# Kernel optimization log

Measured on AMD Instinct MI355X. Metric: run time of the kernel, lower is better.

Reference implementation:

```python
import jax, jax.numpy as jnp
import numpy as np

B, S, H, E, V = 64, 2048, 1024, 512, 32000


def setup_inputs() -> dict:
    key = jax.random.key(0)
    ks = jax.random.split(key, 10)
    s = lambda k, shape, scale: jax.random.normal(k, shape, jnp.float32) * scale
    return {
        "input_batch": jax.random.randint(ks[0], (B,), 0, V),
        "prev_h": s(ks[1], (B, H), 0.1),
        "prev_c": s(ks[2], (B, H), 0.1),
        "encoder_outputs": s(ks[3], (S, B, H), 0.1),
        "emb_W": s(ks[4], (V, E), 0.02),           # nn.Embedding weight
        "attn_W": s(ks[5], (2 * H,), 0.02),        # nn.Linear(2H, 1) weight (flattened)
        "attn_b": jnp.zeros((), jnp.float32),
        "W_ih": s(ks[6], (4 * H, E + H), 0.02),    # LSTMCell weight_ih
        "W_hh": s(ks[7], (4 * H, H), 0.02),        # LSTMCell weight_hh
        "b_ih": jnp.zeros((4 * H,), jnp.float32),
        "b_hh": jnp.zeros((4 * H,), jnp.float32),
        "out_W": s(ks[8], (V, H), 0.02),           # linear_out weight
        "out_b": jnp.zeros((V,), jnp.float32),
    }


def reference(input_batch, prev_h, prev_c, encoder_outputs, emb_W, attn_W, attn_b,
              W_ih, W_hh, b_ih, b_hh, out_W, out_b):
    hid = prev_h.shape[1]
    emb = emb_W[input_batch]                                   # [B, E]

    # Additive attention score attn(cat(prev_h[i], enc[j,i])) vectorized:
    # score[b, s] = prev_h[b] . W[:H] + enc[s, b] . W[H:] + bias
    Wh, We = attn_W[:hid], attn_W[hid:]
    scores = (prev_h @ Wh)[:, None] + jnp.einsum("sbh,h->bs", encoder_outputs, We) + attn_b
    attn_weights = jax.nn.softmax(scores, axis=1)              # [B, S]

    # context = bmm(attn[B,1,S], enc^T[B,S,H]) -> [B, H]
    context = jnp.einsum("bs,sbh->bh", attn_weights, encoder_outputs)

    x = jnp.concatenate([emb, context], axis=1)                # [B, E+H]

    # LSTMCell step (PyTorch gate order: i, f, g, o)
    gates = x @ W_ih.T + b_ih + prev_h @ W_hh.T + b_hh         # [B, 4H]
    i, f, g, o = jnp.split(gates, 4, axis=1)
    i, f, o = jax.nn.sigmoid(i), jax.nn.sigmoid(f), jax.nn.sigmoid(o)
    g = jnp.tanh(g)
    cell = f * prev_c + i * g
    hidden = o * jnp.tanh(cell)

    logits = hidden @ out_W.T + out_b                          # [B, V]
    output = jax.nn.log_softmax(logits, axis=1)
    return output, hidden, cell, attn_weights
```

## Files before the change

kernel.cpp:

```cpp
#include <hip/hip_runtime.h>
#include <math.h>

#define B 64
#define S 2048
#define H 1024
#define E 512
#define V 32000
#define G4 4096
#define KX 1536
#define KC 2560

typedef __attribute__((ext_vector_type(8))) short short8v;
typedef __attribute__((ext_vector_type(4))) float f32x4;

__device__ __forceinline__ ushort f2bf(float f) {
    union { float f; unsigned u; } v; v.f = f;
    unsigned r = v.u + 0x7FFFu + ((v.u >> 16) & 1u);
    return (ushort)(r >> 16);
}

__global__ __launch_bounds__(256) void prep_kernel(const int* __restrict__ ib,
                                                   const float* __restrict__ emb_W,
                                                   const float* __restrict__ prev_h,
                                                   const float* __restrict__ attn_W,
                                                   float* __restrict__ hwh,
                                                   float* __restrict__ xT) {
    __shared__ float red[256];
    int t = threadIdx.x;
    if (blockIdx.x < 64) {
        int b = blockIdx.x;
        float4 p = *(const float4*)(prev_h + b * H + t * 4);
        float4 w = *(const float4*)(attn_W + t * 4);
        red[t] = p.x * w.x + p.y * w.y + p.z * w.z + p.w * w.w;
        __syncthreads();
        for (int s2 = 128; s2; s2 >>= 1) {
            if (t < s2) red[t] += red[t + s2];
            __syncthreads();
        }
        if (t == 0) hwh[b] = red[0];
    } else {
        int g = (blockIdx.x - 64) * 256 + t;
        if (g < E * B) {
            int b = g & 63, k = g >> 6;
            xT[k * B + b] = emb_W[(size_t)ib[b] * E + k];
        } else {
            int g2 = g - E * B;
            int b = g2 & 63, k = g2 >> 6;
            xT[(KX + k) * B + b] = prev_h[b * H + k];
        }
    }
}

__global__ __launch_bounds__(256) void fused_attn_kernel(const float* __restrict__ enc,
                                                         const float* __restrict__ attn_W,
                                                         const float* __restrict__ attn_b,
                                                         const float* __restrict__ hwh,
                                                         float* __restrict__ scores,
                                                         float* __restrict__ cpart,
                                                         float* __restrict__ mlc) {
    __shared__ float mw[4], lw[4];
    __shared__ float cbuf[4][1024];
    int t = threadIdx.x;
    int lane = t & 63, wid = t >> 6;
    int bx = blockIdx.x;
    int b = bx >> 5, chunk = bx & 31;
    int s0 = chunk * 64 + wid * 16;

    const float* We = attn_W + H;
    float4 we4[4];
#pragma unroll
    for (int c = 0; c < 4; ++c) we4[c] = *(const float4*)(We + c * 256 + lane * 4);
    float cst = hwh[b] + attn_b[0];

    float m = -INFINITY, l = 0.f;
    float4 ctx4[4] = {{0,0,0,0},{0,0,0,0},{0,0,0,0},{0,0,0,0}};

    const float* rowp = enc + (size_t)s0 * (B * H) + b * H + lane * 4;
    float4 e4[4];
#pragma unroll
    for (int c = 0; c < 4; ++c) e4[c] = *(const float4*)(rowp + c * 256);

    for (int i = 0; i < 16; ++i) {
        float4 cur[4];
#pragma unroll
        for (int c = 0; c < 4; ++c) cur[c] = e4[c];
        if (i < 15) {
            const float* np = rowp + (size_t)(i + 1) * (B * H);
#pragma unroll
            for (int c = 0; c < 4; ++c) e4[c] = *(const float4*)(np + c * 256);
        }
        float acc = 0.f;
#pragma unroll
        for (int c = 0; c < 4; ++c)
            acc += cur[c].x * we4[c].x + cur[c].y * we4[c].y +
                   cur[c].z * we4[c].z + cur[c].w * we4[c].w;
#pragma unroll
        for (int x = 32; x; x >>= 1) acc += __shfl_xor(acc, x);
        float score = acc + cst;
        if (lane == 0) scores[b * S + s0 + i] = score;
        float nm = fmaxf(m, score);
        float sc = expf(m - nm);
        float w = expf(score - nm);
        l = l * sc + w;
        m = nm;
#pragma unroll
        for (int c = 0; c < 4; ++c) {
            ctx4[c].x = ctx4[c].x * sc + w * cur[c].x;
            ctx4[c].y = ctx4[c].y * sc + w * cur[c].y;
            ctx4[c].z = ctx4[c].z * sc + w * cur[c].z;
            ctx4[c].w = ctx4[c].w * sc + w * cur[c].w;
        }
    }

    if (lane == 0) { mw[wid] = m; lw[wid] = l; }
    __syncthreads();
    float M = fmaxf(fmaxf(mw[0], mw[1]), fmaxf(mw[2], mw[3]));
    float L = lw[0] * expf(mw[0] - M) + lw[1] * expf(mw[1] - M) +
              lw[2] * expf(mw[2] - M) + lw[3] * expf(mw[3] - M);
    float msc = expf(m - M);
#pragma unroll
    for (int c = 0; c < 4; ++c) {
        float4 v = ctx4[c];
        v.x *= msc; v.y *= msc; v.z *= msc; v.w *= msc;
        *(float4*)&cbuf[wid][c * 256 + lane * 4] = v;
    }
    __syncthreads();
    if (wid == 0) {
#pragma unroll
        for (int c = 0; c < 4; ++c) {
            int h = c * 256 + lane * 4;
            float4 a0 = *(float4*)&cbuf[0][h];
            float4 a1 = *(float4*)&cbuf[1][h];
            float4 a2 = *(float4*)&cbuf[2][h];
            float4 a3 = *(float4*)&cbuf[3][h];
            float4 s4 = make_float4(a0.x + a1.x + a2.x + a3.x,
                                    a0.y + a1.y + a2.y + a3.y,
                                    a0.z + a1.z + a2.z + a3.z,
                                    a0.w + a1.w + a2.w + a3.w);
            *(float4*)(cpart + (size_t)(chunk * B + b) * H + h) = s4;
        }
    }
    if (t == 0) {
        mlc[(b * 32 + chunk) * 2] = M;
        mlc[(b * 32 + chunk) * 2 + 1] = L;
    }
}

__global__ __launch_bounds__(256) void attn_reduce_kernel(const float* __restrict__ cpart,
                                                          const float* __restrict__ mlc,
                                                          const float* __restrict__ scores,
                                                          float* __restrict__ xT,
                                                          float* __restrict__ mlf,
                                                          float* __restrict__ attn) {
    __shared__ float Ms[32], Ls[32];
    int b = blockIdx.x, t = threadIdx.x;
    if (t < 32) {
        Ms[t] = mlc[(b * 32 + t) * 2];
        Ls[t] = mlc[(b * 32 + t) * 2 + 1];
    }
    __syncthreads();
    float Mg = -INFINITY;
#pragma unroll
    for (int c = 0; c < 32; ++c) Mg = fmaxf(Mg, Ms[c]);
    float Lg = 0.f;
#pragma unroll
    for (int c = 0; c < 32; ++c) Lg += Ls[c] * expf(Ms[c] - Mg);
    float inv = 1.f / Lg;
    int h = t * 4;
    float4 acc = {0, 0, 0, 0};
    for (int c = 0; c < 32; ++c) {
        float w = expf(Ms[c] - Mg);
        float4 v = *(const float4*)(cpart + (size_t)(c * B + b) * H + h);
        acc.x += w * v.x; acc.y += w * v.y; acc.z += w * v.z; acc.w += w * v.w;
    }
    xT[(E + h) * B + b]     = acc.x * inv;
    xT[(E + h + 1) * B + b] = acc.y * inv;
    xT[(E + h + 2) * B + b] = acc.z * inv;
    xT[(E + h + 3) * B + b] = acc.w * inv;
    if (t == 0) { mlf[b * 2] = Mg; mlf[b * 2 + 1] = Lg; }
#pragma unroll
    for (int i = 0; i < 8; ++i) {
        int s = t + i * 256;
        attn[b * S + s] = expf(scores[b * S + s] - Mg) * inv;
    }
}

__global__ __launch_bounds__(256) void gates_gemm(const float* __restrict__ W_ih,
                                                  const float* __restrict__ W_hh,
                                                  const float* __restrict__ xT,
                                                  float* __restrict__ gpart) {
    __shared__ float Wt[64][68];
    __shared__ float Xt[64][68];
    int t = threadIdx.x;
    int rtile = blockIdx.x >> 3, ks = blockIdx.x & 7;
    int r0 = rtile * 64;
    int rr0 = (t >> 4) * 4;
    int c0 = (t & 15) * 4;
    int sv = t >> 4;
    int sk = (t & 15) * 4;
    float acc[4][4] = {{0.f}};
    for (int kt = 0; kt < 5; ++kt) {
        int kb = ks * 320 + kt * 64;
        const float* wbase;
        int wstride;
        if (kb < KX) { wbase = W_ih + kb; wstride = KX; }
        else         { wbase = W_hh + (kb - KX); wstride = H; }
        __syncthreads();
#pragma unroll
        for (int g = 0; g < 4; ++g) {
            int vv = sv + g * 16;
            *(float4*)&Wt[vv][sk] = *(const float4*)(wbase + (size_t)(r0 + vv) * wstride + sk);
            *(float4*)&Xt[vv][sk] = *(const float4*)(xT + (size_t)(kb + vv) * B + sk);
        }
        __syncthreads();
#pragma unroll
        for (int k0 = 0; k0 < 64; k0 += 4) {
            float w[4][4], x[4][4];
#pragma unroll
            for (int ri = 0; ri < 4; ++ri) *(float4*)w[ri] = *(const float4*)&Wt[rr0 + ri][k0];
#pragma unroll
            for (int kj = 0; kj < 4; ++kj) *(float4*)x[kj] = *(const float4*)&Xt[k0 + kj][c0];
#pragma unroll
            for (int kj = 0; kj < 4; ++kj)
#pragma unroll
                for (int ri = 0; ri < 4; ++ri)
#pragma unroll
                    for (int ci = 0; ci < 4; ++ci)
                        acc[ri][ci] += w[ri][kj] * x[kj][ci];
        }
    }
#pragma unroll
    for (int ri = 0; ri < 4; ++ri) {
        float4 o4 = make_float4(acc[ri][0], acc[ri][1], acc[ri][2], acc[ri][3]);
        *(float4*)(gpart + (size_t)ks * (G4 * B) + (size_t)(r0 + rr0 + ri) * B + c0) = o4;
    }
}

__global__ __launch_bounds__(256) void lstm_kernel(const float* __restrict__ gpart,
                                                   const float* __restrict__ b_ih,
                                                   const float* __restrict__ b_hh,
                                                   const float* __restrict__ prev_c,
                                                   float* __restrict__ hidden_out,
                                                   float* __restrict__ cell_out,
                                                   ushort* __restrict__ hb) {
    int t = blockIdx.x * 256 + threadIdx.x;
    int b = t & 63, h = t >> 6;
    float g[4];
#pragma unroll
    for (int q = 0; q < 4; ++q) {
        int r = h + q * H;
        float a = b_ih[r] + b_hh[r];
#pragma unroll
        for (int ks = 0; ks < 8; ++ks) a += gpart[(size_t)ks * (G4 * B) + r * B + b];
        g[q] = a;
    }
    float ig = 1.f / (1.f + expf(-g[0]));
    float fg = 1.f / (1.f + expf(-g[1]));
    float gg = tanhf(g[2]);
    float og = 1.f / (1.f + expf(-g[3]));
    float c = fg * prev_c[b * H + h] + ig * gg;
    float hd = og * tanhf(c);
    cell_out[b * H + h] = c;
    hidden_out[b * H + h] = hd;
    hb[b * H + h] = f2bf(hd);
}

__global__ __launch_bounds__(256) void logits_mfma(const float* __restrict__ W,
                                                   const float* __restrict__ ob,
                                                   const ushort* __restrict__ hb,
                                                   float* __restrict__ outl) {
    __shared__ ushort Wt[64 * 64];
    __shared__ ushort Bt[64 * 64];
    __shared__ float  Ct[64][68];
    int t = threadIdx.x;
    int lane = t & 63, wid = t >> 6;
    int v0 = blockIdx.x * 64;

    int srow = t >> 2;
    int sq = t & 3;

    f32x4 acc[4] = {{0.f,0.f,0.f,0.f},{0.f,0.f,0.f,0.f},{0.f,0.f,0.f,0.f},{0.f,0.f,0.f,0.f}};

    int r = lane & 15, g = lane >> 4;
    int arow = wid * 16 + r;
    int aswz = (arow & 7) << 4;
    unsigned abase = arow * 128;

    for (int kt = 0; kt < 16; ++kt) {
        int k0 = kt * 64;
        __syncthreads();
        {
            const float* src = W + (size_t)(v0 + srow) * H + k0 + sq * 16;
            float4 f0 = *(const float4*)(src + 0);
            float4 f1 = *(const float4*)(src + 4);
            float4 f2 = *(const float4*)(src + 8);
            float4 f3 = *(const float4*)(src + 12);
            short8v w0, w1;
            w0[0] = (short)f2bf(f0.x); w0[1] = (short)f2bf(f0.y);
            w0[2] = (short)f2bf(f0.z); w0[3] = (short)f2bf(f0.w);
            w0[4] = (short)f2bf(f1.x); w0[5] = (short)f2bf(f1.y);
            w0[6] = (short)f2bf(f1.z); w0[7] = (short)f2bf(f1.w);
            w1[0] = (short)f2bf(f2.x); w1[1] = (short)f2bf(f2.y);
            w1[2] = (short)f2bf(f2.z); w1[3] = (short)f2bf(f2.w);
            w1[4] = (short)f2bf(f3.x); w1[5] = (short)f2bf(f3.y);
            w1[6] = (short)f2bf(f3.z); w1[7] = (short)f2bf(f3.w);
            unsigned rb = srow * 128;
            unsigned sw = (srow & 7) << 4;
            *(short8v*)((char*)Wt + rb + ((sq * 32 + 0) ^ sw))  = w0;
            *(short8v*)((char*)Wt + rb + ((sq * 32 + 16) ^ sw)) = w1;
        }
        {
            const ushort* hsrc = hb + (size_t)srow * H + k0 + sq * 16;
            uint4 h0 = *(const uint4*)(hsrc);
            uint4 h1 = *(const uint4*)(hsrc + 8);
            unsigned rb = srow * 128;
            unsigned sw = (srow & 7) << 4;
            *(uint4*)((char*)Bt + rb + ((sq * 32 + 0) ^ sw))  = h0;
            *(uint4*)((char*)Bt + rb + ((sq * 32 + 16) ^ sw)) = h1;
        }
        __syncthreads();
#pragma unroll
        for (int kk = 0; kk < 2; ++kk) {
            unsigned koff = kk * 64 + g * 16;
            short8v a = *(short8v*)((char*)Wt + abase + (koff ^ aswz));
#pragma unroll
            for (int bt = 0; bt < 4; ++bt) {
                int brow = bt * 16 + r;
                short8v bb = *(short8v*)((char*)Bt + brow * 128 + (koff ^ ((brow & 7) << 4)));
                acc[bt] = __builtin_amdgcn_mfma_f32_16x16x32_bf16(a, bb, acc[bt], 0, 0, 0);
            }
        }
    }
    __syncthreads();
    float bias[4];
#pragma unroll
    for (int j = 0; j < 4; ++j) bias[j] = ob[v0 + wid * 16 + g * 4 + j];
#pragma unroll
    for (int bt = 0; bt < 4; ++bt)
#pragma unroll
        for (int j = 0; j < 4; ++j)
            Ct[bt * 16 + r][wid * 16 + g * 4 + j] = acc[bt][j] + bias[j];
    __syncthreads();
    int ob_ = t >> 2;
    int vq = (t & 3) * 16;
#pragma unroll
    for (int c = 0; c < 4; ++c)
        *(float4*)(outl + (size_t)ob_ * V + v0 + vq + c * 4) = *(float4*)&Ct[ob_][vq + c * 4];
}

__global__ __launch_bounds__(256) void lse_kernel(const float* __restrict__ lg,
                                                  float* __restrict__ c) {
    __shared__ float rm[256], rl[256];
    int b = blockIdx.x, t = threadIdx.x;
    const float4* row = (const float4*)(lg + (size_t)b * V);
    float m = -3.4e38f, l = 0.f;
    for (int i = t; i < V / 4; i += 256) {
        float4 x = row[i];
        float xm = fmaxf(fmaxf(x.x, x.y), fmaxf(x.z, x.w));
        float nm = fmaxf(m, xm);
        l = l * expf(m - nm) + expf(x.x - nm) + expf(x.y - nm) + expf(x.z - nm) + expf(x.w - nm);
        m = nm;
    }
    rm[t] = m; rl[t] = l; __syncthreads();
    for (int s2 = 128; s2; s2 >>= 1) {
        if (t < s2) {
            float m2 = rm[t + s2], l2 = rl[t + s2];
            float nm = fmaxf(rm[t], m2);
            rl[t] = rl[t] * expf(rm[t] - nm) + l2 * expf(m2 - nm);
            rm[t] = nm;
        }
        __syncthreads();
    }
    if (t == 0) c[b] = rm[0] + logf(rl[0]);
}

__global__ __launch_bounds__(256) void lsub_kernel(const float* __restrict__ c,
                                                   float* __restrict__ lg) {
    int g = blockIdx.x * 256 + threadIdx.x;
    int b = g / (V / 4), w = g - b * (V / 4);
    float4* p = (float4*)(lg + (size_t)b * V) + w;
    float4 x = *p;
    float cc = c[b];
    x.x -= cc; x.y -= cc; x.z -= cc; x.w -= cc;
    *p = x;
}

extern "C" void kernel_launch(void* const* d_in, const int* in_sizes, int n_in,
                              void* d_out, int out_size, void* d_ws, size_t ws_size,
                              hipStream_t stream) {
    const int*   ib      = (const int*)d_in[0];
    const float* prev_h  = (const float*)d_in[1];
    const float* prev_c  = (const float*)d_in[2];
    const float* enc     = (const float*)d_in[3];
    const float* emb_W   = (const float*)d_in[4];
    const float* attn_W  = (const float*)d_in[5];
    const float* attn_b  = (const float*)d_in[6];
    const float* W_ih    = (const float*)d_in[7];
    const float* W_hh    = (const float*)d_in[8];
    const float* b_ih    = (const float*)d_in[9];
    const float* b_hh    = (const float*)d_in[10];
    const float* out_W   = (const float*)d_in[11];
    const float* out_b   = (const float*)d_in[12];

    float* ws = (float*)d_ws;
    float* sc   = ws;
    float* hwh  = ws + 131072;
    float* xT   = ws + 131200;
    float* cp   = ws + 295040;
    float* gp   = cp;
    float* mlc  = ws + 2392192;
    float* mlf  = ws + 2396288;
    float* cvec = ws + 2396416;
    ushort* hb  = (ushort*)(ws + 2396480);

    float* out    = (float*)d_out;
    float* out_ls = out;
    float* out_h  = out + (size_t)B * V;
    float* out_c  = out_h + (size_t)B * H;
    float* out_a  = out_c + (size_t)B * H;

    hipLaunchKernelGGL(prep_kernel,        dim3(448),  dim3(256), 0, stream, ib, emb_W, prev_h, attn_W, hwh, xT);
    hipLaunchKernelGGL(fused_attn_kernel,  dim3(2048), dim3(256), 0, stream, enc, attn_W, attn_b, hwh, sc, cp, mlc);
    hipLaunchKernelGGL(attn_reduce_kernel, dim3(B),    dim3(256), 0, stream, cp, mlc, sc, xT, mlf, out_a);
    hipLaunchKernelGGL(gates_gemm,         dim3(512),  dim3(256), 0, stream, W_ih, W_hh, xT, gp);
    hipLaunchKernelGGL(lstm_kernel,        dim3(256),  dim3(256), 0, stream, gp, b_ih, b_hh, prev_c, out_h, out_c, hb);
    hipLaunchKernelGGL(logits_mfma,        dim3(500),  dim3(256), 0, stream, out_W, out_b, hb, out_ls);
    hipLaunchKernelGGL(lse_kernel,         dim3(B),    dim3(256), 0, stream, out_ls, cvec);
    hipLaunchKernelGGL(lsub_kernel,        dim3(2000), dim3(256), 0, stream, cvec, out_ls);
}
```

Measured before the change: 208.2 us.

## Fuse log-softmax partials into logits GEMM, widen attention reduce, use nontemporal loads

```diff
diff --git a/kernel.cpp b/kernel.cpp
--- a/kernel.cpp
+++ b/kernel.cpp
@@ -9,6 +9,7 @@
 #define G4 4096
 #define KX 1536
 #define KC 2560
+#define NVT 500
 
 typedef __attribute__((ext_vector_type(8))) short short8v;
 typedef __attribute__((ext_vector_type(4))) float f32x4;
@@ -17,6 +18,11 @@
     union { float f; unsigned u; } v; v.f = f;
     unsigned r = v.u + 0x7FFFu + ((v.u >> 16) & 1u);
     return (ushort)(r >> 16);
+}
+
+__device__ __forceinline__ float4 ntload4(const float* p) {
+    f32x4 v = __builtin_nontemporal_load((const f32x4*)p);
+    return make_float4(v[0], v[1], v[2], v[3]);
 }
 
 __global__ __launch_bounds__(256) void prep_kernel(const int* __restrict__ ib,
@@ -78,7 +84,7 @@
     const float* rowp = enc + (size_t)s0 * (B * H) + b * H + lane * 4;
     float4 e4[4];
 #pragma unroll
-    for (int c = 0; c < 4; ++c) e4[c] = *(const float4*)(rowp + c * 256);
+    for (int c = 0; c < 4; ++c) e4[c] = ntload4(rowp + c * 256);
 
     for (int i = 0; i < 16; ++i) {
         float4 cur[4];
@@ -87,7 +93,7 @@
         if (i < 15) {
             const float* np = rowp + (size_t)(i + 1) * (B * H);
 #pragma unroll
-            for (int c = 0; c < 4; ++c) e4[c] = *(const float4*)(np + c * 256);
+            for (int c = 0; c < 4; ++c) e4[c] = ntload4(np + c * 256);
         }
         float acc = 0.f;
 #pragma unroll
@@ -150,10 +156,11 @@
                                                           const float* __restrict__ mlc,
                                                           const float* __restrict__ scores,
                                                           float* __restrict__ xT,
-                                                          float* __restrict__ mlf,
                                                           float* __restrict__ attn) {
-    __shared__ float Ms[32], Ls[32];
-    int b = blockIdx.x, t = threadIdx.x;
+    __shared__ float Ms[32], Ls[32], Es[32];
+    int blk = blockIdx.x;
+    int b = blk >> 2, q = blk & 3;
+    int t = threadIdx.x;
     if (t < 32) {
         Ms[t] = mlc[(b * 32 + t) * 2];
         Ls[t] = mlc[(b * 32 + t) * 2 + 1];
@@ -162,25 +169,21 @@
     float Mg = -INFINITY;
 #pragma unroll
     for (int c = 0; c < 32; ++c) Mg = fmaxf(Mg, Ms[c]);
+    if (t < 32) Es[t] = expf(Ms[t] - Mg);
+    __syncthreads();
     float Lg = 0.f;
 #pragma unroll
-    for (int c = 0; c < 32; ++c) Lg += Ls[c] * expf(Ms[c] - Mg);
+    for (int c = 0; c < 32; ++c) Lg += Ls[c] * Es[c];
     float inv = 1.f / Lg;
-    int h = t * 4;
-    float4 acc = {0, 0, 0, 0};
-    for (int c = 0; c < 32; ++c) {
-        float w = expf(Ms[c] - Mg);
-        float4 v = *(const float4*)(cpart + (size_t)(c * B + b) * H + h);
-        acc.x += w * v.x; acc.y += w * v.y; acc.z += w * v.z; acc.w += w * v.w;
-    }
-    xT[(E + h) * B + b]     = acc.x * inv;
-    xT[(E + h + 1) * B + b] = acc.y * inv;
-    xT[(E + h + 2) * B + b] = acc.z * inv;
-    xT[(E + h + 3) * B + b] = acc.w * inv;
-    if (t == 0) { mlf[b * 2] = Mg; mlf[b * 2 + 1] = Lg; }
-#pragma unroll
-    for (int i = 0; i < 8; ++i) {
-        int s = t + i * 256;
+    int h = q * 256 + t;
+    float acc = 0.f;
+#pragma unroll 4
+    for (int c = 0; c < 32; ++c)
+        acc += Es[c] * cpart[(size_t)(c * B + b) * H + h];
+    xT[(E + h) * B + b] = acc * inv;
+#pragma unroll
+    for (int i = 0; i < 2; ++i) {
+        int s = q * 512 + i * 256 + t;
         attn[b * S + s] = expf(scores[b * S + s] - Mg) * inv;
     }
 }
@@ -268,7 +271,8 @@
 __global__ __launch_bounds__(256) void logits_mfma(const float* __restrict__ W,
                                                    const float* __restrict__ ob,
                                                    const ushort* __restrict__ hb,
-                                                   float* __restrict__ outl) {
+                                                   float* __restrict__ outl,
+                                                   float* __restrict__ lsp) {
     __shared__ ushort Wt[64 * 64];
     __shared__ ushort Bt[64 * 64];
     __shared__ float  Ct[64][68];
@@ -291,10 +295,10 @@
         __syncthreads();
         {
             const float* src = W + (size_t)(v0 + srow) * H + k0 + sq * 16;
-            float4 f0 = *(const float4*)(src + 0);
-            float4 f1 = *(const float4*)(src + 4);
-            float4 f2 = *(const float4*)(src + 8);
-            float4 f3 = *(const float4*)(src + 12);
+            float4 f0 = ntload4(src + 0);
+            float4 f1 = ntload4(src + 4);
+            float4 f2 = ntload4(src + 8);
+            float4 f3 = ntload4(src + 12);
             short8v w0, w1;
             w0[0] = (short)f2bf(f0.x); w0[1] = (short)f2bf(f0.y);
             w0[2] = (short)f2bf(f0.z); w0[3] = (short)f2bf(f0.w);
@@ -343,22 +347,46 @@
     __syncthreads();
     int ob_ = t >> 2;
     int vq = (t & 3) * 16;
+    float4 vals[4];
+    float pm = -3.4e38f;
+#pragma unroll
+    for (int c = 0; c < 4; ++c) {
+        vals[c] = *(float4*)&Ct[ob_][vq + c * 4];
+        pm = fmaxf(pm, fmaxf(fmaxf(vals[c].x, vals[c].y), fmaxf(vals[c].z, vals[c].w)));
+        *(float4*)(outl + (size_t)ob_ * V + v0 + vq + c * 4) = vals[c];
+    }
+    float ps = 0.f;
 #pragma unroll
     for (int c = 0; c < 4; ++c)
-        *(float4*)(outl + (size_t)ob_ * V + v0 + vq + c * 4) = *(float4*)&Ct[ob_][vq + c * 4];
-}
-
-__global__ __launch_bounds__(256) void lse_kernel(const float* __restrict__ lg,
-                                                  float* __restrict__ c) {
+        ps += expf(vals[c].x - pm) + expf(vals[c].y - pm) +
+              expf(vals[c].z - pm) + expf(vals[c].w - pm);
+#pragma unroll
+    for (int x = 1; x <= 2; x <<= 1) {
+        float om = __shfl_xor(pm, x);
+        float os = __shfl_xor(ps, x);
+        float nm = fmaxf(pm, om);
+        ps = ps * expf(pm - nm) + os * expf(om - nm);
+        pm = nm;
+    }
+    if ((t & 3) == 0) {
+        lsp[((size_t)ob_ * NVT + blockIdx.x) * 2]     = pm;
+        lsp[((size_t)ob_ * NVT + blockIdx.x) * 2 + 1] = ps;
+    }
+}
+
+__global__ __launch_bounds__(256) void lsub_kernel(const float* __restrict__ lsp,
+                                                   float* __restrict__ lg) {
     __shared__ float rm[256], rl[256];
-    int b = blockIdx.x, t = threadIdx.x;
-    const float4* row = (const float4*)(lg + (size_t)b * V);
-    float m = -3.4e38f, l = 0.f;
-    for (int i = t; i < V / 4; i += 256) {
-        float4 x = row[i];
-        float xm = fmaxf(fmaxf(x.x, x.y), fmaxf(x.z, x.w));
-        float nm = fmaxf(m, xm);
-        l = l * expf(m - nm) + expf(x.x - nm) + expf(x.y - nm) + expf(x.z - nm) + expf(x.w - nm);
+    int blk = blockIdx.x;
+    int b = blk >> 5, chunk = blk & 31;
+    int t = threadIdx.x;
+    const float* pb = lsp + (size_t)b * (NVT * 2);
+    float m = pb[t * 2], l = pb[t * 2 + 1];
+    int i2 = t + 256;
+    if (i2 < NVT) {
+        float m1 = pb[i2 * 2], l1 = pb[i2 * 2 + 1];
+        float nm = fmaxf(m, m1);
+        l = l * expf(m - nm) + l1 * expf(m1 - nm);
         m = nm;
     }
     rm[t] = m; rl[t] = l; __syncthreads();
@@ -371,18 +399,13 @@
         }
         __syncthreads();
     }
-    if (t == 0) c[b] = rm[0] + logf(rl[0]);
-}
-
-__global__ __launch_bounds__(256) void lsub_kernel(const float* __restrict__ c,
-                                                   float* __restrict__ lg) {
-    int g = blockIdx.x * 256 + threadIdx.x;
-    int b = g / (V / 4), w = g - b * (V / 4);
-    float4* p = (float4*)(lg + (size_t)b * V) + w;
-    float4 x = *p;
-    float cc = c[b];
-    x.x -= cc; x.y -= cc; x.z -= cc; x.w -= cc;
-    *p = x;
+    float c = rm[0] + logf(rl[0]);
+    if (t < 250) {
+        float4* p = (float4*)(lg + (size_t)b * V + chunk * 1000) + t;
+        float4 x = *p;
+        x.x -= c; x.y -= c; x.z -= c; x.w -= c;
+        *p = x;
+    }
 }
 
 extern "C" void kernel_launch(void* const* d_in, const int* in_sizes, int n_in,
@@ -409,9 +432,8 @@
     float* cp   = ws + 295040;
     float* gp   = cp;
     float* mlc  = ws + 2392192;
-    float* mlf  = ws + 2396288;
-    float* cvec = ws + 2396416;
-    ushort* hb  = (ushort*)(ws + 2396480);
+    ushort* hb  = (ushort*)(ws + 2396288);
+    float* lsp  = ws + 2429056;
 
     float* out    = (float*)d_out;
     float* out_ls = out;
@@ -421,10 +443,9 @@
 
     hipLaunchKernelGGL(prep_kernel,        dim3(448),  dim3(256), 0, stream, ib, emb_W, prev_h, attn_W, hwh, xT);
     hipLaunchKernelGGL(fused_attn_kernel,  dim3(2048), dim3(256), 0, stream, enc, attn_W, attn_b, hwh, sc, cp, mlc);
-    hipLaunchKernelGGL(attn_reduce_kernel, dim3(B),    dim3(256), 0, stream, cp, mlc, sc, xT, mlf, out_a);
+    hipLaunchKernelGGL(attn_reduce_kernel, dim3(256),  dim3(256), 0, stream, cp, mlc, sc, xT, out_a);
     hipLaunchKernelGGL(gates_gemm,         dim3(512),  dim3(256), 0, stream, W_ih, W_hh, xT, gp);
     hipLaunchKernelGGL(lstm_kernel,        dim3(256),  dim3(256), 0, stream, gp, b_ih, b_hh, prev_c, out_h, out_c, hb);
-    hipLaunchKernelGGL(logits_mfma,        dim3(500),  dim3(256), 0, stream, out_W, out_b, hb, out_ls);
-    hipLaunchKernelGGL(lse_kernel,         dim3(B),    dim3(256), 0, stream, out_ls, cvec);
-    hipLaunchKernelGGL(lsub_kernel,        dim3(2000), dim3(256), 0, stream, cvec, out_ls);
-}
+    hipLaunchKernelGGL(logits_mfma,        dim3(NVT),  dim3(256), 0, stream, out_W, out_b, hb, out_ls, lsp);
+    hipLaunchKernelGGL(lsub_kernel,        dim3(2048), dim3(256), 0, stream, lsp, out_ls);
+}
```

New measurement: 184.3 us. 1.13x faster.
